# Kernel tuning notes

Hardware: AMD Instinct MI355X
Metric: run time of the kernel (lower is better)

Reference implementation:

```python
import jax, jax.numpy as jnp
import numpy as np

CELL = 0.5          # grid_map cell size (meters)
NUM_POSES = 256     # config.num_pose_samples


def setup_inputs() -> dict:
    key = jax.random.key(0)
    k1, k2, k3, k4 = jax.random.split(key, 4)
    B, N, I, J, D = 2, 1024, 128, 128, 32
    f_q = jax.random.normal(k1, (B, N, D), jnp.float32)
    f_map = jax.random.normal(k2, (B, I, J, D), jnp.float32)
    # query frustum points: 32x32 grid, x in [-15.5, 15.5], y in [0.5, 31.5]
    xs = jnp.arange(32, dtype=jnp.float32) - 15.5
    ys = jnp.arange(32, dtype=jnp.float32) + 0.5
    grid = jnp.stack(jnp.meshgrid(xs, ys, indexing='ij'), -1).reshape(-1, 2)
    q_xy = jnp.broadcast_to(grid, (B, N, 2)).astype(jnp.float32)
    valid_q = jax.random.bernoulli(k3, 0.9, (B, N))
    valid_map = jax.random.bernoulli(k4, 0.8, (B, I, J))
    temperature = jnp.array(0.5, jnp.float32)
    return {"f_q": f_q, "f_map": f_map, "q_xy": q_xy, "temperature": temperature,
            "valid_q": valid_q, "valid_map": valid_map, "seed": 0}


def reference(f_q, f_map, q_xy, temperature, valid_q, valid_map, seed):
    B, N, D = f_q.shape
    _, I, J, _ = f_map.shape
    K = NUM_POSES

    # dense cross-correlation: [B, N, I, J]
    sim = jnp.einsum('bnd,bijd->bnij', f_q, f_map)
    sim = jax.nn.relu(sim)                      # clip_negative_scores
    sim = sim.astype(jnp.float32) * jnp.exp(temperature)
    # joint softmax over the two spatial axes
    m = sim.max(axis=(-2, -1), keepdims=True)
    e = jnp.exp(sim - m)
    prob = e / e.sum(axis=(-2, -1), keepdims=True)
    num_valid = valid_q.sum(-1).clip(min=1).astype(jnp.float32)[:, None, None, None]
    sim = sim / num_valid
    prob = prob / num_valid

    # --- RANSAC 2-point pose sampling (no gradient through prob) ---
    p = jax.lax.stop_gradient(prob)
    kq, km = jax.random.split(jax.random.key(seed))
    n_idx = jax.random.randint(kq, (B, 2 * K), 0, N)          # 2 query pts per pose
    b_idx = jnp.arange(B)[:, None]
    p_flat = p.reshape(B, N, I * J)
    rows = p_flat[b_idx, n_idx]                               # [B, 2K, IJ]
    m_flat = jax.random.categorical(km, jnp.log(rows + 1e-20), axis=-1)  # [B, 2K]
    mi, mj = m_flat // J, m_flat % J
    m_xy = (jnp.stack([mi, mj], -1).astype(jnp.float32) + 0.5) * CELL    # cell centers
    m_xy = m_xy.reshape(B, K, 2, 2)
    q_pts = q_xy[b_idx, n_idx].reshape(B, K, 2, 2)
    dq = q_pts[:, :, 1] - q_pts[:, :, 0]
    dm = m_xy[:, :, 1] - m_xy[:, :, 0]
    theta = jnp.arctan2(dm[..., 1], dm[..., 0]) - jnp.arctan2(dq[..., 1], dq[..., 0])
    c, s = jnp.cos(theta), jnp.sin(theta)
    R = jnp.stack([jnp.stack([c, -s], -1), jnp.stack([s, c], -1)], -2)   # [B,K,2,2]
    t = m_xy[:, :, 0] - jnp.einsum('bkxy,bky->bkx', R, q_pts[:, :, 0])   # [B,K,2]

    # --- score every pose hypothesis ---
    p_map = jnp.einsum('bkxy,bny->bknx', R, q_xy) + t[:, :, None]        # [B,K,N,2]
    ij = jnp.floor(p_map / CELL).astype(jnp.int32)
    inb = (ij[..., 0] >= 0) & (ij[..., 0] < I) & (ij[..., 1] >= 0) & (ij[..., 1] < J)
    flat = jnp.clip(ij[..., 0], 0, I - 1) * J + jnp.clip(ij[..., 1], 0, J - 1)  # [B,K,N]
    vmap_flat = valid_map.reshape(B, I * J)
    vgather = vmap_flat[b_idx, flat.reshape(B, K * N)].reshape(B, K, N)
    sim_flat = sim.reshape(B, N, I * J)
    sgather = jnp.take_along_axis(sim_flat, flat.transpose(0, 2, 1), axis=2)  # [B,N,K]
    mask = valid_q[:, None, :] & inb & vgather                                # [B,K,N]
    scores = jnp.sum(sgather.transpose(0, 2, 1) * mask, axis=-1)              # [B,K]
    return scores
```

## Files before the change

kernel.cpp:

```cpp
#include <hip/hip_runtime.h>
#include <stdint.h>

typedef unsigned int u32;
typedef unsigned long long u64;
typedef _Float16 f16x8 __attribute__((ext_vector_type(8)));
typedef _Float16 f16x4 __attribute__((ext_vector_type(4)));
typedef float f32x4 __attribute__((ext_vector_type(4)));

#define IJ 16384
#define NQ 1024
#define NB 2
#define KP 256
#define NSEG 16
#define SEGW 1024
#define NT 1024

__device__ __forceinline__ void tf2x32(u32 k0, u32 k1, u32& x0, u32& x1) {
  u32 kx = k0 ^ k1 ^ 0x1BD11BDAu;
#define TFR(r) { x0 += x1; x1 = (x1 << (r)) | (x1 >> (32 - (r))); x1 ^= x0; }
  x0 += k0; x1 += k1;
  TFR(13) TFR(15) TFR(26) TFR(6)
  x0 += k1; x1 += kx + 1u;
  TFR(17) TFR(29) TFR(16) TFR(24)
  x0 += kx; x1 += k0 + 2u;
  TFR(13) TFR(15) TFR(26) TFR(6)
  x0 += k0; x1 += k1 + 3u;
  TFR(17) TFR(29) TFR(16) TFR(24)
  x0 += k1; x1 += kx + 4u;
  TFR(13) TFR(15) TFR(26) TFR(6)
  x0 += kx; x1 += k0 + 5u;
#undef TFR
}

__device__ __forceinline__ void tf_subkey(u32 k0, u32 k1, u32 i, u32& s0, u32& s1) {
  u32 x0 = 0u, x1 = i;
  tf2x32(k0, k1, x0, x1);
  s0 = x0; s1 = x1;
}

__device__ __forceinline__ u32 tf_xorbits(u32 k0, u32 k1, u32 i) {
  u32 x0 = 0u, x1 = i;
  tf2x32(k0, k1, x0, x1);
  return x0 ^ x1;
}

__device__ __forceinline__ void derive_keys(int seed, u32& kq0, u32& kq1,
                                            u32& km0, u32& km1) {
  u32 k0 = 0u;
  u32 k1 = (u32)seed;
  tf_subkey(k0, k1, 0u, kq0, kq1);
  tf_subkey(k0, k1, 1u, km0, km1);
}

__device__ __forceinline__ float gumbel_from_bits(u32 w) {
  const float tiny = 1.17549435e-38f;
  float fl = __uint_as_float((w >> 9) | 0x3f800000u) - 1.0f;
  float u = fl * (1.0f - tiny) + tiny;
  u = fmaxf(tiny, u);
  return -logf(-logf(u));
}

__device__ __forceinline__ bool read_bool(const void* p, int idx, int is32) {
  return is32 ? (((const int*)p)[idx] != 0)
              : (((const unsigned char*)p)[idx] != 0);
}

__device__ __forceinline__ u32 fkey(float x) {
  u32 b = __float_as_uint(x);
  return b ^ ((b & 0x80000000u) ? 0xFFFFFFFFu : 0x80000000u);
}
__device__ __forceinline__ float fkey_inv(u32 k) {
  u32 b = k ^ ((k & 0x80000000u) ? 0x80000000u : 0xFFFFFFFFu);
  return __uint_as_float(b);
}

__device__ __forceinline__ void split8(const float* x, f16x8& h1, f16x8& h2) {
#pragma unroll
  for (int e = 0; e < 8; ++e) {
    _Float16 a = (_Float16)x[e];
    h1[e] = a;
    h2[e] = (_Float16)((x[e] - (float)a) * 2048.0f);
  }
}

__global__ void setup_kernel(const void* __restrict__ valid_q,
                             const int* __restrict__ seedp,
                             const float* __restrict__ f_q,
                             const float* __restrict__ f_map,
                             float* __restrict__ tmax,
                             float* __restrict__ num_valid,
                             int* __restrict__ n_idx,
                             int* __restrict__ bool_is32,
                             _Float16* __restrict__ ms1,
                             _Float16* __restrict__ ms2,
                             _Float16* __restrict__ qs1,
                             _Float16* __restrict__ qs2) {
  __shared__ int sred[256];
  __shared__ int is32_s;
  const int blk = blockIdx.x, tid = threadIdx.x;
  if (blk < 4) {
    int s = blk * 256 + tid;
    u32 kq0, kq1, km0, km1;
    derive_keys(seedp[0], kq0, kq1, km0, km1);
    u32 l0, l1;
    tf_subkey(kq0, kq1, 1u, l0, l1);
    u32 w = tf_xorbits(l0, l1, (u32)s);
    n_idx[s] = (int)(w & 1023u);
  } else if (blk == 4) {
    const unsigned char* vb = (const unsigned char*)valid_q;
    int ones = 0;
    for (int i = tid; i < 2048; i += 256) ones += (vb[i] == 1) ? 1 : 0;
    sred[tid] = ones;
    __syncthreads();
    for (int off = 128; off > 0; off >>= 1) {
      if (tid < off) sred[tid] += sred[tid + off];
      __syncthreads();
    }
    if (tid == 0) {
      is32_s = (sred[0] < 1152) ? 1 : 0;
      bool_is32[0] = is32_s;
    }
    __syncthreads();
    const int is32 = is32_s;
    for (int b = 0; b < 2; ++b) {
      int acc = 0;
      for (int i = tid; i < NQ; i += 256)
        acc += read_bool(valid_q, b * NQ + i, is32) ? 1 : 0;
      sred[tid] = acc;
      __syncthreads();
      for (int off = 128; off > 0; off >>= 1) {
        if (tid < off) sred[tid] += sred[tid + off];
        __syncthreads();
      }
      if (tid == 0) {
        float nv = (float)sred[0];
        num_valid[b] = nv < 1.f ? 1.f : nv;
      }
      __syncthreads();
    }
  } else if (blk < 8) {
    for (int i = (blk - 5) * 256 + tid; i < NT; i += 768) tmax[i] = 0.f;
  } else if (blk < 520) {
    const int TT = (blk - 8) * 4 + (tid >> 6);
    const int l = tid & 63;
    const int bb = TT >> 10, T = TT & 1023;
    const float* src =
        f_map + ((size_t)bb * IJ + T * 16 + (l & 15)) * 32 + ((l >> 4) << 2);
    float4 v0 = *(const float4*)src;
    float4 v1 = *(const float4*)(src + 16);
    float x[8] = {v0.x, v0.y, v0.z, v0.w, v1.x, v1.y, v1.z, v1.w};
    f16x8 h1, h2;
    split8(x, h1, h2);
    *(f16x8*)(ms1 + (size_t)(TT * 64 + l) * 8) = h1;
    *(f16x8*)(ms2 + (size_t)(TT * 64 + l) * 8) = h2;
  } else {
    const int i = (blk - 520) * 256 + tid;
    const float* src = f_q + (size_t)i * 8;
    float4 a = *(const float4*)src;
    float4 b4 = *(const float4*)(src + 4);
    float x[8] = {a.x, a.y, a.z, a.w, b4.x, b4.y, b4.z, b4.w};
    f16x8 h1, h2;
    split8(x, h1, h2);
    *(f16x8*)(qs1 + (size_t)i * 8) = h1;
    *(f16x8*)(qs2 + (size_t)i * 8) = h2;
  }
}

__global__ __launch_bounds__(256) void stats_kernel(
    const _Float16* __restrict__ ms1, const _Float16* __restrict__ ms2,
    const _Float16* __restrict__ qs1, const _Float16* __restrict__ qs2,
    const int* __restrict__ n_idx, const float* __restrict__ temp,
    float* __restrict__ tmax, float* __restrict__ rowsum_part) {
  const int bx = blockIdx.x;
  const int by = blockIdx.y;
  const int tid = threadIdx.x;
  const int w = tid >> 6, l = tid & 63, l15 = l & 15, g = l >> 4;
  const int b = by >> 3;
  const int tp = by * 64 + w * 16 + l15;
  const int n = n_idx[tp];
  const size_t qb = ((size_t)b * NQ + n) * 32 + g * 4;
  union { f16x8 v8; f16x4 v4[2]; } uq;
  uq.v4[0] = *(const f16x4*)(qs1 + qb);
  uq.v4[1] = *(const f16x4*)(qs1 + qb + 16);
  const f16x8 q1 = uq.v8;
  uq.v4[0] = *(const f16x4*)(qs2 + qb);
  uq.v4[1] = *(const f16x4*)(qs2 + qb + 16);
  const f16x8 q2 = uq.v8;
  const float et = expf(temp[0]);
  const f32x4 zero4 = {0.f, 0.f, 0.f, 0.f};
  const float c11 = 4.8828125e-4f;
  const size_t mbase = ((size_t)b * 1024 + bx * 16) * 512 + (size_t)l * 8;
  float rm = 0.f, se = 0.f;
#pragma unroll
  for (int T = 0; T < 16; ++T) {
    const f16x8 m1 = *(const f16x8*)(ms1 + mbase + (size_t)T * 512);
    const f16x8 m2 = *(const f16x8*)(ms2 + mbase + (size_t)T * 512);
    f32x4 x = __builtin_amdgcn_mfma_f32_16x16x32_f16(m2, q2, zero4, 0, 0, 0);
    x *= c11;
    x = __builtin_amdgcn_mfma_f32_16x16x32_f16(m2, q1, x, 0, 0, 0);
    x = __builtin_amdgcn_mfma_f32_16x16x32_f16(m1, q2, x, 0, 0, 0);
    x *= c11;
    f32x4 r = __builtin_amdgcn_mfma_f32_16x16x32_f16(m1, q1, x, 0, 0, 0);
#pragma unroll
    for (int j = 0; j < 4; ++j) {
      float v = fmaxf(r[j], 0.f) * et;
      rm = fmaxf(rm, v);
      se += __expf(v);
    }
  }
  se += __shfl_xor(se, 16, 64);
  rm = fmaxf(rm, __shfl_xor(rm, 16, 64));
  se += __shfl_xor(se, 32, 64);
  rm = fmaxf(rm, __shfl_xor(rm, 32, 64));
  if (g == 0) {
    rowsum_part[(size_t)tp * 64 + bx] = se;
    atomicMax((u32*)&tmax[tp], __float_as_uint(rm));
  }
}

__global__ void sumexp_reduce_kernel(const float* __restrict__ rowsum_part,
                                     const float* __restrict__ tmax,
                                     float* __restrict__ tsum) {
  const int row = blockIdx.x * 256 + threadIdx.x;
  if (row >= NT) return;
  const float* p = rowsum_part + (size_t)row * 64;
  float s = 0.f;
#pragma unroll
  for (int t = 0; t < 64; ++t) s += p[t];
  tsum[row] = s * expf(-tmax[row]);
}

__global__ __launch_bounds__(256) void select_kernel(
    const _Float16* __restrict__ ms1, const _Float16* __restrict__ ms2,
    const _Float16* __restrict__ qs1, const _Float16* __restrict__ qs2,
    const int* __restrict__ n_idx, const float* __restrict__ temp,
    const float* __restrict__ tmax, const float* __restrict__ tsum,
    const float* __restrict__ num_valid, const int* __restrict__ seedp,
    float* __restrict__ segv, int* __restrict__ segi) {
  __shared__ float mrow[16], srow[16];
  __shared__ u64 best[16];
  __shared__ u32 keysm[2];
  __shared__ int cnt;
  __shared__ u32 candk[4096];
  __shared__ float candv[4096];
  const int seg = blockIdx.x;
  const int tg = blockIdx.y;
  const int tid = threadIdx.x;
  const int w = tid >> 6, l = tid & 63, l15 = l & 15, g = l >> 4;
  const int b = tg >> 5;
  const int t0 = tg * 16;
  if (tid < 16) {
    mrow[tid] = tmax[t0 + tid];
    srow[tid] = tsum[t0 + tid];
    best[tid] = ((u64)fkey(-1e30f) << 32) | (u64)(0xFFFFFFFFu - (u32)IJ);
  }
  if (tid == 0) {
    u32 kq0, kq1, km0, km1;
    derive_keys(seedp[0], kq0, kq1, km0, km1);
    keysm[0] = km0; keysm[1] = km1;
    cnt = 0;
  }
  const int tp = t0 + l15;
  const int n = n_idx[tp];
  const size_t qb = ((size_t)b * NQ + n) * 32 + g * 4;
  union { f16x8 v8; f16x4 v4[2]; } uq;
  uq.v4[0] = *(const f16x4*)(qs1 + qb);
  uq.v4[1] = *(const f16x4*)(qs1 + qb + 16);
  const f16x8 q1 = uq.v8;
  uq.v4[0] = *(const f16x4*)(qs2 + qb);
  uq.v4[1] = *(const f16x4*)(qs2 + qb + 16);
  const f16x8 q2 = uq.v8;
  const float et = expf(temp[0]);
  const f32x4 zero4 = {0.f, 0.f, 0.f, 0.f};
  const float c11 = 4.8828125e-4f;
  const float nv = num_valid[b];
  __syncthreads();
  const float th = mrow[l15] - 25.0f;
  const u32 km0 = keysm[0], km1 = keysm[1];

  for (int sc = 0; sc < 4; ++sc) {
#pragma unroll
    for (int i = 0; i < 4; ++i) {
      const int Tl = sc * 16 + w * 4 + i;
      const size_t moff = ((size_t)(b * 1024 + seg * 64 + Tl) * 64 + l) * 8;
      const f16x8 m1 = *(const f16x8*)(ms1 + moff);
      const f16x8 m2 = *(const f16x8*)(ms2 + moff);
      f32x4 x = __builtin_amdgcn_mfma_f32_16x16x32_f16(m2, q2, zero4, 0, 0, 0);
      x *= c11;
      x = __builtin_amdgcn_mfma_f32_16x16x32_f16(m2, q1, x, 0, 0, 0);
      x = __builtin_amdgcn_mfma_f32_16x16x32_f16(m1, q2, x, 0, 0, 0);
      x *= c11;
      f32x4 r = __builtin_amdgcn_mfma_f32_16x16x32_f16(m1, q1, x, 0, 0, 0);
#pragma unroll
      for (int j = 0; j < 4; ++j) {
        float v = fmaxf(r[j], 0.f) * et;
        if (v > th) {
          int p = atomicAdd(&cnt, 1);
          candk[p] = ((u32)l15 << 12) | (u32)(Tl * 16 + g * 4 + j);
          candv[p] = v;
        }
      }
    }
    __syncthreads();
    const int C = cnt;
    for (int c = tid; c < C; c += 256) {
      const u32 e = candk[c];
      const int r = (int)(e >> 12);
      const int f = seg * SEGW + (int)(e & 4095u);
      const float val = candv[c];
      const u32 wb = tf_xorbits(km0, km1, (u32)((t0 + r) * IJ + f));
      const float gmb = gumbel_from_bits(wb);
      const float v = logf((expf(val - mrow[r]) / srow[r]) / nv + 1e-20f) + gmb;
      const u64 key = ((u64)fkey(v) << 32) | (u64)(0xFFFFFFFFu - (u32)f);
      atomicMax(&best[r], key);
    }
    __syncthreads();
    if (tid == 0) cnt = 0;
    __syncthreads();
  }
  if (tid < 16) {
    const u64 k = best[tid];
    segv[(size_t)(t0 + tid) * NSEG + seg] = fkey_inv((u32)(k >> 32));
    segi[(size_t)(t0 + tid) * NSEG + seg] =
        (int)(0xFFFFFFFFu - (u32)(k & 0xFFFFFFFFu));
  }
}

__global__ void cat_reduce_kernel(const float* __restrict__ segv,
                                  const int* __restrict__ segi,
                                  int* __restrict__ m_flat) {
  const int idx = blockIdx.x * 256 + threadIdx.x;
  if (idx >= NT) return;
  float bv = -1e30f;
  int bi = IJ;
#pragma unroll
  for (int s = 0; s < NSEG; ++s) {
    float v = segv[idx * NSEG + s];
    int i = segi[idx * NSEG + s];
    if (v > bv || (v == bv && i < bi)) { bv = v; bi = i; }
  }
  m_flat[idx] = bi;
}

__global__ void pose_kernel(const float* __restrict__ q_xy,
                            const int* __restrict__ n_idx,
                            const int* __restrict__ m_flat,
                            float4* __restrict__ poses) {
  const int idx = blockIdx.x * 256 + threadIdx.x;
  if (idx >= NB * KP) return;
  const int b = idx >> 8, k = idx & 255;
  const int t0 = b * 512 + 2 * k, t1 = t0 + 1;
  const int na = n_idx[t0], nb = n_idx[t1];
  const float2 q0 = ((const float2*)q_xy)[(size_t)b * NQ + na];
  const float2 q1 = ((const float2*)q_xy)[(size_t)b * NQ + nb];
  const int ma = m_flat[t0], mb = m_flat[t1];
  const float m0x = ((float)(ma >> 7) + 0.5f) * 0.5f;
  const float m0y = ((float)(ma & 127) + 0.5f) * 0.5f;
  const float m1x = ((float)(mb >> 7) + 0.5f) * 0.5f;
  const float m1y = ((float)(mb & 127) + 0.5f) * 0.5f;
  const float dqx = q1.x - q0.x, dqy = q1.y - q0.y;
  const float dmx = m1x - m0x, dmy = m1y - m0y;
  const float theta = atan2f(dmy, dmx) - atan2f(dqy, dqx);
  const float c = cosf(theta), s = sinf(theta);
  const float tx = m0x - (c * q0.x - s * q0.y);
  const float ty = m0y - (s * q0.x + c * q0.y);
  poses[idx] = make_float4(c, s, tx, ty);
}

__global__ __launch_bounds__(256) void score_kernel(
    const float* __restrict__ f_q, const float* __restrict__ f_map,
    const float* __restrict__ q_xy, const void* __restrict__ valid_q,
    const void* __restrict__ valid_map, const float* __restrict__ num_valid,
    const float* __restrict__ temp, const float4* __restrict__ poses,
    const int* __restrict__ bool_is32, float* __restrict__ out) {
  __shared__ float sred[256];
  const int idx = blockIdx.x;
  const int tid = threadIdx.x;
  const int b = idx >> 8;
  const int is32 = bool_is32[0];
  const float4 P = poses[idx];
  const float et = expf(temp[0]);
  float acc = 0.f;
  for (int n = tid; n < NQ; n += 256) {
    float2 q = ((const float2*)q_xy)[(size_t)b * NQ + n];
    float px = P.x * q.x - P.y * q.y + P.z;
    float py = P.y * q.x + P.x * q.y + P.w;
    int ii = (int)floorf(px * 2.0f);
    int jj = (int)floorf(py * 2.0f);
    bool inb = (ii >= 0) & (ii < 128) & (jj >= 0) & (jj < 128);
    int ic = min(max(ii, 0), 127), jc = min(max(jj, 0), 127);
    int flat = (ic << 7) + jc;
    bool msk = read_bool(valid_q, b * NQ + n, is32) && inb &&
               read_bool(valid_map, b * IJ + flat, is32);
    if (msk) {
      const float4* A = (const float4*)(f_q + ((size_t)b * NQ + n) * 32);
      const float4* Bm = (const float4*)(f_map + ((size_t)b * IJ + flat) * 32);
      float4 s4 = {0.f, 0.f, 0.f, 0.f};
#pragma unroll
      for (int r = 0; r < 8; ++r) {
        float4 a = A[r], bb = Bm[r];
        s4.x = fmaf(a.x, bb.x, s4.x);
        s4.y = fmaf(a.y, bb.y, s4.y);
        s4.z = fmaf(a.z, bb.z, s4.z);
        s4.w = fmaf(a.w, bb.w, s4.w);
      }
      float dot = (s4.x + s4.y) + (s4.z + s4.w);
      acc += fmaxf(dot, 0.f) * et;
    }
  }
  sred[tid] = acc;
  __syncthreads();
  for (int off = 128; off > 0; off >>= 1) {
    if (tid < off) sred[tid] += sred[tid + off];
    __syncthreads();
  }
  if (tid == 0) out[idx] = sred[0] / num_valid[b];
}

extern "C" void kernel_launch(void* const* d_in, const int* in_sizes, int n_in,
                              void* d_out, int out_size, void* d_ws,
                              size_t ws_size, hipStream_t stream) {
  const float* f_q = (const float*)d_in[0];
  const float* f_map = (const float*)d_in[1];
  const float* q_xy = (const float*)d_in[2];
  const float* temp = (const float*)d_in[3];
  const void* valid_q = d_in[4];
  const void* valid_map = d_in[5];
  const int* seedp = (const int*)d_in[6];
  float* out = (float*)d_out;

  char* ws = (char*)d_ws;
  _Float16* ms1 = (_Float16*)(ws + 0);
  _Float16* ms2 = (_Float16*)(ws + 2097152);
  _Float16* qs1 = (_Float16*)(ws + 4194304);
  _Float16* qs2 = (_Float16*)(ws + 4325376);
  float* tmax = (float*)(ws + 4456448);
  float* tsum = (float*)(ws + 4460544);
  float* rowsum_part = (float*)(ws + 4464640);
  float* num_valid = (float*)(ws + 4726784);
  int* n_idx = (int*)(ws + 4726848);
  int* m_flat = (int*)(ws + 4730944);
  float4* poses = (float4*)(ws + 4735040);
  int* bool_is32 = (int*)(ws + 4743232);
  float* segv = (float*)(ws + 4743296);
  int* segi = (int*)(ws + 4808832);

  setup_kernel<<<552, 256, 0, stream>>>(valid_q, seedp, f_q, f_map, tmax,
                                        num_valid, n_idx, bool_is32, ms1, ms2,
                                        qs1, qs2);
  stats_kernel<<<dim3(64, 16), 256, 0, stream>>>(ms1, ms2, qs1, qs2, n_idx,
                                                 temp, tmax, rowsum_part);
  sumexp_reduce_kernel<<<4, 256, 0, stream>>>(rowsum_part, tmax, tsum);
  select_kernel<<<dim3(NSEG, 64), 256, 0, stream>>>(
      ms1, ms2, qs1, qs2, n_idx, temp, tmax, tsum, num_valid, seedp, segv,
      segi);
  cat_reduce_kernel<<<4, 256, 0, stream>>>(segv, segi, m_flat);
  pose_kernel<<<2, 256, 0, stream>>>(q_xy, n_idx, m_flat, poses);
  score_kernel<<<NB * KP, 256, 0, stream>>>(f_q, f_map, q_xy, valid_q,
                                            valid_map, num_valid, temp, poses,
                                            bool_is32, out);
}
```

Baseline: 144.9 us.

## Fuse pipeline into three kernels with on-the-fly fp16 splitting and global atomic argmax

Removes the setup pre-pass that split f_q/f_map into fp16 hi/lo buffers; the stats and select kernels now load fp32 and split in registers. The sumexp, cat_reduce and pose kernels are folded in: per-chunk maxima are reduced inside select, the categorical argmax is combined through a global 64-bit atomicMax, and score_kernel derives the pose itself. n_idx is recomputed with Threefry wherever needed. This trims launches and buffer traffic at the cost of redundant split and RNG arithmetic. The pruning threshold also tightens from 25 to 22, and best is zeroed inside a stats block while select writes it, which relies on kernel ordering.

```diff
diff --git a/kernel.cpp b/kernel.cpp
--- a/kernel.cpp
+++ b/kernel.cpp
@@ -4,7 +4,6 @@
 typedef unsigned int u32;
 typedef unsigned long long u64;
 typedef _Float16 f16x8 __attribute__((ext_vector_type(8)));
-typedef _Float16 f16x4 __attribute__((ext_vector_type(4)));
 typedef float f32x4 __attribute__((ext_vector_type(4)));
 
 #define IJ 16384
@@ -52,6 +51,14 @@
   tf_subkey(k0, k1, 1u, km0, km1);
 }
 
+__device__ __forceinline__ int derive_n(int seed, u32 s) {
+  u32 kq0, kq1, km0, km1;
+  derive_keys(seed, kq0, kq1, km0, km1);
+  u32 l0, l1;
+  tf_subkey(kq0, kq1, 1u, l0, l1);
+  return (int)(tf_xorbits(l0, l1, s) & 1023u);
+}
+
 __device__ __forceinline__ float gumbel_from_bits(u32 w) {
   const float tiny = 1.17549435e-38f;
   float fl = __uint_as_float((w >> 9) | 0x3f800000u) - 1.0f;
@@ -69,44 +76,75 @@
   u32 b = __float_as_uint(x);
   return b ^ ((b & 0x80000000u) ? 0xFFFFFFFFu : 0x80000000u);
 }
-__device__ __forceinline__ float fkey_inv(u32 k) {
-  u32 b = k ^ ((k & 0x80000000u) ? 0x80000000u : 0xFFFFFFFFu);
-  return __uint_as_float(b);
-}
-
-__device__ __forceinline__ void split8(const float* x, f16x8& h1, f16x8& h2) {
+
+__device__ __forceinline__ void load_split(const float* __restrict__ src,
+                                           f16x8& h1, f16x8& h2) {
+  float4 a = *(const float4*)src;
+  float4 b = *(const float4*)(src + 16);
+  float x[8] = {a.x, a.y, a.z, a.w, b.x, b.y, b.z, b.w};
 #pragma unroll
   for (int e = 0; e < 8; ++e) {
-    _Float16 a = (_Float16)x[e];
-    h1[e] = a;
-    h2[e] = (_Float16)((x[e] - (float)a) * 2048.0f);
-  }
-}
-
-__global__ void setup_kernel(const void* __restrict__ valid_q,
-                             const int* __restrict__ seedp,
-                             const float* __restrict__ f_q,
-                             const float* __restrict__ f_map,
-                             float* __restrict__ tmax,
-                             float* __restrict__ num_valid,
-                             int* __restrict__ n_idx,
-                             int* __restrict__ bool_is32,
-                             _Float16* __restrict__ ms1,
-                             _Float16* __restrict__ ms2,
-                             _Float16* __restrict__ qs1,
-                             _Float16* __restrict__ qs2) {
+    _Float16 hi = (_Float16)x[e];
+    h1[e] = hi;
+    h2[e] = (_Float16)((x[e] - (float)hi) * 2048.0f);
+  }
+}
+
+__device__ __forceinline__ f32x4 emul_mfma(f16x8 m1, f16x8 m2, f16x8 q1,
+                                           f16x8 q2) {
+  const f32x4 zero4 = {0.f, 0.f, 0.f, 0.f};
+  const float c11 = 4.8828125e-4f;
+  f32x4 x = __builtin_amdgcn_mfma_f32_16x16x32_f16(m2, q2, zero4, 0, 0, 0);
+  x *= c11;
+  x = __builtin_amdgcn_mfma_f32_16x16x32_f16(m2, q1, x, 0, 0, 0);
+  x = __builtin_amdgcn_mfma_f32_16x16x32_f16(m1, q2, x, 0, 0, 0);
+  x *= c11;
+  return __builtin_amdgcn_mfma_f32_16x16x32_f16(m1, q1, x, 0, 0, 0);
+}
+
+__global__ __launch_bounds__(256) void stats_kernel(
+    const float* __restrict__ f_q, const float* __restrict__ f_map,
+    const float* __restrict__ temp, const void* __restrict__ valid_q,
+    const int* __restrict__ seedp, float* __restrict__ chunkmax,
+    float* __restrict__ rowsum_part, u64* __restrict__ best,
+    float* __restrict__ num_valid, int* __restrict__ bool_is32) {
   __shared__ int sred[256];
   __shared__ int is32_s;
-  const int blk = blockIdx.x, tid = threadIdx.x;
-  if (blk < 4) {
-    int s = blk * 256 + tid;
-    u32 kq0, kq1, km0, km1;
-    derive_keys(seedp[0], kq0, kq1, km0, km1);
-    u32 l0, l1;
-    tf_subkey(kq0, kq1, 1u, l0, l1);
-    u32 w = tf_xorbits(l0, l1, (u32)s);
-    n_idx[s] = (int)(w & 1023u);
-  } else if (blk == 4) {
+  const int bx = blockIdx.x;
+  const int by = blockIdx.y;
+  const int tid = threadIdx.x;
+  const int w = tid >> 6, l = tid & 63, l15 = l & 15, g = l >> 4;
+  const int b = by >> 3;
+  const int tp = by * 64 + w * 16 + l15;
+  const int n = derive_n(seedp[0], (u32)tp);
+  f16x8 q1, q2;
+  load_split(f_q + ((size_t)b * NQ + n) * 32 + g * 4, q1, q2);
+  const float et = expf(temp[0]);
+  float rm = 0.f, se = 0.f;
+#pragma unroll
+  for (int T = 0; T < 16; ++T) {
+    f16x8 m1, m2;
+    load_split(f_map + ((size_t)b * IJ + (bx * 16 + T) * 16 + l15) * 32 + g * 4,
+               m1, m2);
+    f32x4 r = emul_mfma(m1, m2, q1, q2);
+#pragma unroll
+    for (int j = 0; j < 4; ++j) {
+      float v = fmaxf(r[j], 0.f) * et;
+      rm = fmaxf(rm, v);
+      se += __expf(v);
+    }
+  }
+  se += __shfl_xor(se, 16, 64);
+  rm = fmaxf(rm, __shfl_xor(rm, 16, 64));
+  se += __shfl_xor(se, 32, 64);
+  rm = fmaxf(rm, __shfl_xor(rm, 32, 64));
+  if (g == 0) {
+    chunkmax[(size_t)tp * 64 + bx] = rm;
+    rowsum_part[(size_t)tp * 64 + bx] = se;
+  }
+  if (bx == 0 && by == 0) {
+    __syncthreads();
+    for (int i = tid; i < NT; i += 256) best[i] = 0ull;
     const unsigned char* vb = (const unsigned char*)valid_q;
     int ones = 0;
     for (int i = tid; i < 2048; i += 256) ones += (vb[i] == 1) ? 1 : 0;
@@ -122,10 +160,10 @@
     }
     __syncthreads();
     const int is32 = is32_s;
-    for (int b = 0; b < 2; ++b) {
+    for (int bb = 0; bb < 2; ++bb) {
       int acc = 0;
       for (int i = tid; i < NQ; i += 256)
-        acc += read_bool(valid_q, b * NQ + i, is32) ? 1 : 0;
+        acc += read_bool(valid_q, bb * NQ + i, is32) ? 1 : 0;
       sred[tid] = acc;
       __syncthreads();
       for (int off = 128; off > 0; off >>= 1) {
@@ -134,112 +172,20 @@
       }
       if (tid == 0) {
         float nv = (float)sred[0];
-        num_valid[b] = nv < 1.f ? 1.f : nv;
+        num_valid[bb] = nv < 1.f ? 1.f : nv;
       }
       __syncthreads();
     }
-  } else if (blk < 8) {
-    for (int i = (blk - 5) * 256 + tid; i < NT; i += 768) tmax[i] = 0.f;
-  } else if (blk < 520) {
-    const int TT = (blk - 8) * 4 + (tid >> 6);
-    const int l = tid & 63;
-    const int bb = TT >> 10, T = TT & 1023;
-    const float* src =
-        f_map + ((size_t)bb * IJ + T * 16 + (l & 15)) * 32 + ((l >> 4) << 2);
-    float4 v0 = *(const float4*)src;
-    float4 v1 = *(const float4*)(src + 16);
-    float x[8] = {v0.x, v0.y, v0.z, v0.w, v1.x, v1.y, v1.z, v1.w};
-    f16x8 h1, h2;
-    split8(x, h1, h2);
-    *(f16x8*)(ms1 + (size_t)(TT * 64 + l) * 8) = h1;
-    *(f16x8*)(ms2 + (size_t)(TT * 64 + l) * 8) = h2;
-  } else {
-    const int i = (blk - 520) * 256 + tid;
-    const float* src = f_q + (size_t)i * 8;
-    float4 a = *(const float4*)src;
-    float4 b4 = *(const float4*)(src + 4);
-    float x[8] = {a.x, a.y, a.z, a.w, b4.x, b4.y, b4.z, b4.w};
-    f16x8 h1, h2;
-    split8(x, h1, h2);
-    *(f16x8*)(qs1 + (size_t)i * 8) = h1;
-    *(f16x8*)(qs2 + (size_t)i * 8) = h2;
-  }
-}
-
-__global__ __launch_bounds__(256) void stats_kernel(
-    const _Float16* __restrict__ ms1, const _Float16* __restrict__ ms2,
-    const _Float16* __restrict__ qs1, const _Float16* __restrict__ qs2,
-    const int* __restrict__ n_idx, const float* __restrict__ temp,
-    float* __restrict__ tmax, float* __restrict__ rowsum_part) {
-  const int bx = blockIdx.x;
-  const int by = blockIdx.y;
-  const int tid = threadIdx.x;
-  const int w = tid >> 6, l = tid & 63, l15 = l & 15, g = l >> 4;
-  const int b = by >> 3;
-  const int tp = by * 64 + w * 16 + l15;
-  const int n = n_idx[tp];
-  const size_t qb = ((size_t)b * NQ + n) * 32 + g * 4;
-  union { f16x8 v8; f16x4 v4[2]; } uq;
-  uq.v4[0] = *(const f16x4*)(qs1 + qb);
-  uq.v4[1] = *(const f16x4*)(qs1 + qb + 16);
-  const f16x8 q1 = uq.v8;
-  uq.v4[0] = *(const f16x4*)(qs2 + qb);
-  uq.v4[1] = *(const f16x4*)(qs2 + qb + 16);
-  const f16x8 q2 = uq.v8;
-  const float et = expf(temp[0]);
-  const f32x4 zero4 = {0.f, 0.f, 0.f, 0.f};
-  const float c11 = 4.8828125e-4f;
-  const size_t mbase = ((size_t)b * 1024 + bx * 16) * 512 + (size_t)l * 8;
-  float rm = 0.f, se = 0.f;
-#pragma unroll
-  for (int T = 0; T < 16; ++T) {
-    const f16x8 m1 = *(const f16x8*)(ms1 + mbase + (size_t)T * 512);
-    const f16x8 m2 = *(const f16x8*)(ms2 + mbase + (size_t)T * 512);
-    f32x4 x = __builtin_amdgcn_mfma_f32_16x16x32_f16(m2, q2, zero4, 0, 0, 0);
-    x *= c11;
-    x = __builtin_amdgcn_mfma_f32_16x16x32_f16(m2, q1, x, 0, 0, 0);
-    x = __builtin_amdgcn_mfma_f32_16x16x32_f16(m1, q2, x, 0, 0, 0);
-    x *= c11;
-    f32x4 r = __builtin_amdgcn_mfma_f32_16x16x32_f16(m1, q1, x, 0, 0, 0);
-#pragma unroll
-    for (int j = 0; j < 4; ++j) {
-      float v = fmaxf(r[j], 0.f) * et;
-      rm = fmaxf(rm, v);
-      se += __expf(v);
-    }
-  }
-  se += __shfl_xor(se, 16, 64);
-  rm = fmaxf(rm, __shfl_xor(rm, 16, 64));
-  se += __shfl_xor(se, 32, 64);
-  rm = fmaxf(rm, __shfl_xor(rm, 32, 64));
-  if (g == 0) {
-    rowsum_part[(size_t)tp * 64 + bx] = se;
-    atomicMax((u32*)&tmax[tp], __float_as_uint(rm));
-  }
-}
-
-__global__ void sumexp_reduce_kernel(const float* __restrict__ rowsum_part,
-                                     const float* __restrict__ tmax,
-                                     float* __restrict__ tsum) {
-  const int row = blockIdx.x * 256 + threadIdx.x;
-  if (row >= NT) return;
-  const float* p = rowsum_part + (size_t)row * 64;
-  float s = 0.f;
-#pragma unroll
-  for (int t = 0; t < 64; ++t) s += p[t];
-  tsum[row] = s * expf(-tmax[row]);
+  }
 }
 
 __global__ __launch_bounds__(256) void select_kernel(
-    const _Float16* __restrict__ ms1, const _Float16* __restrict__ ms2,
-    const _Float16* __restrict__ qs1, const _Float16* __restrict__ qs2,
-    const int* __restrict__ n_idx, const float* __restrict__ temp,
-    const float* __restrict__ tmax, const float* __restrict__ tsum,
-    const float* __restrict__ num_valid, const int* __restrict__ seedp,
-    float* __restrict__ segv, int* __restrict__ segi) {
+    const float* __restrict__ f_q, const float* __restrict__ f_map,
+    const float* __restrict__ temp, const float* __restrict__ chunkmax,
+    const float* __restrict__ rowsum_part, const float* __restrict__ num_valid,
+    const int* __restrict__ seedp, u64* __restrict__ best) {
   __shared__ float mrow[16], srow[16];
-  __shared__ u64 best[16];
-  __shared__ u32 keysm[2];
+  __shared__ u64 lbest[16];
   __shared__ int cnt;
   __shared__ u32 candk[4096];
   __shared__ float candv[4096];
@@ -249,48 +195,39 @@
   const int w = tid >> 6, l = tid & 63, l15 = l & 15, g = l >> 4;
   const int b = tg >> 5;
   const int t0 = tg * 16;
+  u32 kq0, kq1, km0, km1;
+  derive_keys(seedp[0], kq0, kq1, km0, km1);
   if (tid < 16) {
-    mrow[tid] = tmax[t0 + tid];
-    srow[tid] = tsum[t0 + tid];
-    best[tid] = ((u64)fkey(-1e30f) << 32) | (u64)(0xFFFFFFFFu - (u32)IJ);
-  }
-  if (tid == 0) {
-    u32 kq0, kq1, km0, km1;
-    derive_keys(seedp[0], kq0, kq1, km0, km1);
-    keysm[0] = km0; keysm[1] = km1;
-    cnt = 0;
-  }
-  const int tp = t0 + l15;
-  const int n = n_idx[tp];
-  const size_t qb = ((size_t)b * NQ + n) * 32 + g * 4;
-  union { f16x8 v8; f16x4 v4[2]; } uq;
-  uq.v4[0] = *(const f16x4*)(qs1 + qb);
-  uq.v4[1] = *(const f16x4*)(qs1 + qb + 16);
-  const f16x8 q1 = uq.v8;
-  uq.v4[0] = *(const f16x4*)(qs2 + qb);
-  uq.v4[1] = *(const f16x4*)(qs2 + qb + 16);
-  const f16x8 q2 = uq.v8;
+    const float* cm = chunkmax + (size_t)(t0 + tid) * 64;
+    const float* rp = rowsum_part + (size_t)(t0 + tid) * 64;
+    float m = 0.f;
+#pragma unroll
+    for (int c = 0; c < 64; ++c) m = fmaxf(m, cm[c]);
+    float s = 0.f;
+#pragma unroll
+    for (int c = 0; c < 64; ++c) s += rp[c];
+    mrow[tid] = m;
+    srow[tid] = s * expf(-m);
+    lbest[tid] = 0ull;
+  }
+  if (tid == 0) cnt = 0;
+  const int n = derive_n(seedp[0], (u32)(t0 + l15));
+  f16x8 q1, q2;
+  load_split(f_q + ((size_t)b * NQ + n) * 32 + g * 4, q1, q2);
   const float et = expf(temp[0]);
-  const f32x4 zero4 = {0.f, 0.f, 0.f, 0.f};
-  const float c11 = 4.8828125e-4f;
   const float nv = num_valid[b];
   __syncthreads();
-  const float th = mrow[l15] - 25.0f;
-  const u32 km0 = keysm[0], km1 = keysm[1];
+  const float th = mrow[l15] - 22.0f;
 
   for (int sc = 0; sc < 4; ++sc) {
 #pragma unroll
     for (int i = 0; i < 4; ++i) {
       const int Tl = sc * 16 + w * 4 + i;
-      const size_t moff = ((size_t)(b * 1024 + seg * 64 + Tl) * 64 + l) * 8;
-      const f16x8 m1 = *(const f16x8*)(ms1 + moff);
-      const f16x8 m2 = *(const f16x8*)(ms2 + moff);
-      f32x4 x = __builtin_amdgcn_mfma_f32_16x16x32_f16(m2, q2, zero4, 0, 0, 0);
-      x *= c11;
-      x = __builtin_amdgcn_mfma_f32_16x16x32_f16(m2, q1, x, 0, 0, 0);
-      x = __builtin_amdgcn_mfma_f32_16x16x32_f16(m1, q2, x, 0, 0, 0);
-      x *= c11;
-      f32x4 r = __builtin_amdgcn_mfma_f32_16x16x32_f16(m1, q1, x, 0, 0, 0);
+      f16x8 m1, m2;
+      load_split(
+          f_map + ((size_t)b * IJ + seg * SEGW + Tl * 16 + l15) * 32 + g * 4,
+          m1, m2);
+      f32x4 r = emul_mfma(m1, m2, q1, q2);
 #pragma unroll
       for (int j = 0; j < 4; ++j) {
         float v = fmaxf(r[j], 0.f) * et;
@@ -312,73 +249,50 @@
       const float gmb = gumbel_from_bits(wb);
       const float v = logf((expf(val - mrow[r]) / srow[r]) / nv + 1e-20f) + gmb;
       const u64 key = ((u64)fkey(v) << 32) | (u64)(0xFFFFFFFFu - (u32)f);
-      atomicMax(&best[r], key);
+      atomicMax(&lbest[r], key);
     }
     __syncthreads();
     if (tid == 0) cnt = 0;
     __syncthreads();
   }
-  if (tid < 16) {
-    const u64 k = best[tid];
-    segv[(size_t)(t0 + tid) * NSEG + seg] = fkey_inv((u32)(k >> 32));
-    segi[(size_t)(t0 + tid) * NSEG + seg] =
-        (int)(0xFFFFFFFFu - (u32)(k & 0xFFFFFFFFu));
-  }
-}
-
-__global__ void cat_reduce_kernel(const float* __restrict__ segv,
-                                  const int* __restrict__ segi,
-                                  int* __restrict__ m_flat) {
-  const int idx = blockIdx.x * 256 + threadIdx.x;
-  if (idx >= NT) return;
-  float bv = -1e30f;
-  int bi = IJ;
-#pragma unroll
-  for (int s = 0; s < NSEG; ++s) {
-    float v = segv[idx * NSEG + s];
-    int i = segi[idx * NSEG + s];
-    if (v > bv || (v == bv && i < bi)) { bv = v; bi = i; }
-  }
-  m_flat[idx] = bi;
-}
-
-__global__ void pose_kernel(const float* __restrict__ q_xy,
-                            const int* __restrict__ n_idx,
-                            const int* __restrict__ m_flat,
-                            float4* __restrict__ poses) {
-  const int idx = blockIdx.x * 256 + threadIdx.x;
-  if (idx >= NB * KP) return;
-  const int b = idx >> 8, k = idx & 255;
-  const int t0 = b * 512 + 2 * k, t1 = t0 + 1;
-  const int na = n_idx[t0], nb = n_idx[t1];
-  const float2 q0 = ((const float2*)q_xy)[(size_t)b * NQ + na];
-  const float2 q1 = ((const float2*)q_xy)[(size_t)b * NQ + nb];
-  const int ma = m_flat[t0], mb = m_flat[t1];
-  const float m0x = ((float)(ma >> 7) + 0.5f) * 0.5f;
-  const float m0y = ((float)(ma & 127) + 0.5f) * 0.5f;
-  const float m1x = ((float)(mb >> 7) + 0.5f) * 0.5f;
-  const float m1y = ((float)(mb & 127) + 0.5f) * 0.5f;
-  const float dqx = q1.x - q0.x, dqy = q1.y - q0.y;
-  const float dmx = m1x - m0x, dmy = m1y - m0y;
-  const float theta = atan2f(dmy, dmx) - atan2f(dqy, dqx);
-  const float c = cosf(theta), s = sinf(theta);
-  const float tx = m0x - (c * q0.x - s * q0.y);
-  const float ty = m0y - (s * q0.x + c * q0.y);
-  poses[idx] = make_float4(c, s, tx, ty);
+  if (tid < 16) atomicMax(&best[t0 + tid], lbest[tid]);
 }
 
 __global__ __launch_bounds__(256) void score_kernel(
     const float* __restrict__ f_q, const float* __restrict__ f_map,
     const float* __restrict__ q_xy, const void* __restrict__ valid_q,
     const void* __restrict__ valid_map, const float* __restrict__ num_valid,
-    const float* __restrict__ temp, const float4* __restrict__ poses,
-    const int* __restrict__ bool_is32, float* __restrict__ out) {
+    const float* __restrict__ temp, const u64* __restrict__ best,
+    const int* __restrict__ seedp, const int* __restrict__ bool_is32,
+    float* __restrict__ out) {
   __shared__ float sred[256];
+  __shared__ float4 Psh;
   const int idx = blockIdx.x;
   const int tid = threadIdx.x;
-  const int b = idx >> 8;
+  const int b = idx >> 8, k = idx & 255;
+  if (tid == 0) {
+    const int t0 = b * 512 + 2 * k, t1 = t0 + 1;
+    const int na = derive_n(seedp[0], (u32)t0);
+    const int nb = derive_n(seedp[0], (u32)t1);
+    const float2 q0 = ((const float2*)q_xy)[(size_t)b * NQ + na];
+    const float2 q1 = ((const float2*)q_xy)[(size_t)b * NQ + nb];
+    const int ma = (int)(0xFFFFFFFFu - (u32)(best[t0] & 0xFFFFFFFFu));
+    const int mb = (int)(0xFFFFFFFFu - (u32)(best[t1] & 0xFFFFFFFFu));
+    const float m0x = ((float)(ma >> 7) + 0.5f) * 0.5f;
+    const float m0y = ((float)(ma & 127) + 0.5f) * 0.5f;
+    const float m1x = ((float)(mb >> 7) + 0.5f) * 0.5f;
+    const float m1y = ((float)(mb & 127) + 0.5f) * 0.5f;
+    const float dqx = q1.x - q0.x, dqy = q1.y - q0.y;
+    const float dmx = m1x - m0x, dmy = m1y - m0y;
+    const float theta = atan2f(dmy, dmx) - atan2f(dqy, dqx);
+    const float c = cosf(theta), s = sinf(theta);
+    const float tx = m0x - (c * q0.x - s * q0.y);
+    const float ty = m0y - (s * q0.x + c * q0.y);
+    Psh = make_float4(c, s, tx, ty);
+  }
+  __syncthreads();
+  const float4 P = Psh;
   const int is32 = bool_is32[0];
-  const float4 P = poses[idx];
   const float et = expf(temp[0]);
   float acc = 0.f;
   for (int n = tid; n < NQ; n += 256) {
@@ -430,33 +344,18 @@
   float* out = (float*)d_out;
 
   char* ws = (char*)d_ws;
-  _Float16* ms1 = (_Float16*)(ws + 0);
-  _Float16* ms2 = (_Float16*)(ws + 2097152);
-  _Float16* qs1 = (_Float16*)(ws + 4194304);
-  _Float16* qs2 = (_Float16*)(ws + 4325376);
-  float* tmax = (float*)(ws + 4456448);
-  float* tsum = (float*)(ws + 4460544);
-  float* rowsum_part = (float*)(ws + 4464640);
-  float* num_valid = (float*)(ws + 4726784);
-  int* n_idx = (int*)(ws + 4726848);
-  int* m_flat = (int*)(ws + 4730944);
-  float4* poses = (float4*)(ws + 4735040);
-  int* bool_is32 = (int*)(ws + 4743232);
-  float* segv = (float*)(ws + 4743296);
-  int* segi = (int*)(ws + 4808832);
-
-  setup_kernel<<<552, 256, 0, stream>>>(valid_q, seedp, f_q, f_map, tmax,
-                                        num_valid, n_idx, bool_is32, ms1, ms2,
-                                        qs1, qs2);
-  stats_kernel<<<dim3(64, 16), 256, 0, stream>>>(ms1, ms2, qs1, qs2, n_idx,
-                                                 temp, tmax, rowsum_part);
-  sumexp_reduce_kernel<<<4, 256, 0, stream>>>(rowsum_part, tmax, tsum);
+  float* chunkmax = (float*)ws;
+  float* rowsum_part = (float*)(ws + 262144);
+  u64* best = (u64*)(ws + 524288);
+  float* num_valid = (float*)(ws + 532480);
+  int* bool_is32 = (int*)(ws + 532544);
+
+  stats_kernel<<<dim3(64, 16), 256, 0, stream>>>(
+      f_q, f_map, temp, valid_q, seedp, chunkmax, rowsum_part, best, num_valid,
+      bool_is32);
   select_kernel<<<dim3(NSEG, 64), 256, 0, stream>>>(
-      ms1, ms2, qs1, qs2, n_idx, temp, tmax, tsum, num_valid, seedp, segv,
-      segi);
-  cat_reduce_kernel<<<4, 256, 0, stream>>>(segv, segi, m_flat);
-  pose_kernel<<<2, 256, 0, stream>>>(q_xy, n_idx, m_flat, poses);
+      f_q, f_map, temp, chunkmax, rowsum_part, num_valid, seedp, best);
   score_kernel<<<NB * KP, 256, 0, stream>>>(f_q, f_map, q_xy, valid_q,
-                                            valid_map, num_valid, temp, poses,
-                                            bool_is32, out);
-}
+                                            valid_map, num_valid, temp, best,
+                                            seedp, bool_is32, out);
+}
```

Result: faster. 138.0 us (median of 2 runs) (-4.8%).
